# Performance work log

Hardware: AMD Instinct MI355X
Metric: run time of the kernel (lower is better)

## Reference

```python
import jax, jax.numpy as jnp
import numpy as np

D_MODEL = 1024
NUM_HEADS = 16
HEAD_DIM = D_MODEL // NUM_HEADS


def setup_inputs() -> dict:
    key = jax.random.key(0)
    ks = jax.random.split(key, 9)
    s = 1.0 / np.sqrt(D_MODEL)
    x = jax.random.normal(ks[0], (4, 2048, D_MODEL), dtype=jnp.float32)
    Wq = jax.random.uniform(ks[1], (D_MODEL, D_MODEL), jnp.float32, -s, s)
    bq = jax.random.uniform(ks[2], (D_MODEL,), jnp.float32, -s, s)
    Wk = jax.random.uniform(ks[3], (D_MODEL, D_MODEL), jnp.float32, -s, s)
    bk = jax.random.uniform(ks[4], (D_MODEL,), jnp.float32, -s, s)
    Wv = jax.random.uniform(ks[5], (D_MODEL, D_MODEL), jnp.float32, -s, s)
    bv = jax.random.uniform(ks[6], (D_MODEL,), jnp.float32, -s, s)
    Wo = jax.random.uniform(ks[7], (D_MODEL, D_MODEL), jnp.float32, -s, s)
    bo = jax.random.uniform(ks[8], (D_MODEL,), jnp.float32, -s, s)
    return {"x": x, "Wq": Wq, "bq": bq, "Wk": Wk, "bk": bk,
            "Wv": Wv, "bv": bv, "Wo": Wo, "bo": bo}


def reference(x, Wq, bq, Wk, bk, Wv, bv, Wo, bo):
    B, S, _ = x.shape
    H, Dh = NUM_HEADS, HEAD_DIM
    # projections (torch Linear: x @ W.T + b); split heads -> [B, H, S, Dh]
    q = (x @ Wq.T + bq).reshape(B, S, H, Dh).transpose(0, 2, 1, 3)
    k = (x @ Wk.T + bk).reshape(B, S, H, Dh).transpose(0, 2, 1, 3)
    v = (x @ Wv.T + bv).reshape(B, S, H, Dh).transpose(0, 2, 1, 3)
    scale = 1.0 / np.sqrt(Dh)
    scores = jnp.einsum("bhqd,bhkd->bhqk", q, k) * scale  # [B,H,S,S]
    attn = jax.nn.softmax(scores, axis=-1)
    out = jnp.einsum("bhqk,bhkd->bhqd", attn, v)  # [B,H,S,Dh]
    out = out.transpose(0, 2, 1, 3).reshape(B, S, H * Dh)
    return out @ Wo.T + bo
```

## Files before the change

kernel.cpp:

```cpp
#include <hip/hip_runtime.h>
#include <hip/hip_bf16.h>
#include <stdint.h>

typedef __hip_bfloat16 bf16;
typedef __attribute__((ext_vector_type(8))) short short8;
typedef __attribute__((ext_vector_type(4))) short short4v;
typedef __attribute__((ext_vector_type(4))) float f32x4;

#define MFMA16(a, b, c) __builtin_amdgcn_mfma_f32_16x16x32_bf16(a, b, c, 0, 0, 0)
#define LROW 144

static __device__ __forceinline__ short f2bf(float f) {
    bf16 h = __float2bfloat16(f);
    return *(short*)&h;
}

#define BAR_LGKM() asm volatile("s_waitcnt lgkmcnt(0)\ns_barrier" ::: "memory")
#define BAR_RAW()  asm volatile("s_barrier" ::: "memory")

__global__ __launch_bounds__(256) void cvt_f32_bf16(const float* __restrict__ s,
                                                    bf16* __restrict__ d, int n8) {
    int i = blockIdx.x * blockDim.x + threadIdx.x;
    if (i >= n8) return;
    f32x4 a0 = *(const f32x4*)(s + (size_t)i * 8);
    f32x4 a1 = *(const f32x4*)(s + (size_t)i * 8 + 4);
    short8 r;
#pragma unroll
    for (int j = 0; j < 4; ++j) {
        r[j] = f2bf(a0[j]);
        r[4 + j] = f2bf(a1[j]);
    }
    *(short8*)(d + (size_t)i * 8) = r;
}

template <int MODE, bool SCALE, bool AF32>
__global__ __launch_bounds__(256) void gemm128(const void* __restrict__ Araw,
                                               const void* __restrict__ Wraw,
                                               const float* __restrict__ bias,
                                               void* __restrict__ outraw) {
    __shared__ __align__(16) char As[128 * LROW];
    __shared__ __align__(16) char Bs[128 * LROW];
    const int t = threadIdx.x;
    const int lane = t & 63;
    const int w = t >> 6;
    const int m0 = blockIdx.x * 128;
    const int n0 = blockIdx.y * 128;
    const int wm = (w >> 1) * 64;
    const int wn = (w & 1) * 64;

    f32x4 acc[4][4] = {};
    const char* Ab = (const char*)Araw;
    const char* Wb = (const char*)Wraw;

    short8 av[4], wv[4];
    auto loadAB = [&](int k0) {
#pragma unroll
        for (int i = 0; i < 4; ++i) {
            int off = i * 4096 + t * 16;
            int row = off >> 7;
            int cb = off & 127;
            if (MODE == 3) {
                int gr = m0 + row;
                int bb = gr >> 11, ss = gr & 2047;
                int h = k0 >> 6;
                av[i] = *(const short8*)(Ab +
                        (((size_t)(bb * 16 + h) * 2048 + ss) * 64) * 2 + cb);
            } else if (AF32) {
                const char* s = Ab + (size_t)(m0 + row) * 4096 +
                                (size_t)k0 * 4 + cb * 2;
                f32x4 a0 = *(const f32x4*)s;
                f32x4 a1 = *(const f32x4*)(s + 16);
                short8 r;
#pragma unroll
                for (int j = 0; j < 4; ++j) { r[j] = f2bf(a0[j]); r[4+j] = f2bf(a1[j]); }
                av[i] = r;
            } else {
                av[i] = *(const short8*)(Ab + (size_t)(m0 + row) * 2048 +
                                         (size_t)k0 * 2 + cb);
            }
            if (AF32) {
                const char* s = Wb + (size_t)(n0 + row) * 4096 +
                                (size_t)k0 * 4 + cb * 2;
                f32x4 a0 = *(const f32x4*)s;
                f32x4 a1 = *(const f32x4*)(s + 16);
                short8 r;
#pragma unroll
                for (int j = 0; j < 4; ++j) { r[j] = f2bf(a0[j]); r[4+j] = f2bf(a1[j]); }
                wv[i] = r;
            } else {
                wv[i] = *(const short8*)(Wb + (size_t)(n0 + row) * 2048 +
                                         (size_t)k0 * 2 + cb);
            }
        }
    };

    loadAB(0);
    for (int k0 = 0; k0 < 1024; k0 += 64) {
#pragma unroll
        for (int i = 0; i < 4; ++i) {
            int off = i * 4096 + t * 16;
            int row = off >> 7, cb = off & 127;
            *(short8*)(As + row * LROW + cb) = av[i];
            *(short8*)(Bs + row * LROW + cb) = wv[i];
        }
        if (k0 < 960) loadAB(k0 + 64);
        BAR_LGKM();
#pragma unroll
        for (int kk = 0; kk < 2; ++kk) {
            short8 af[4], bfr[4];
#pragma unroll
            for (int m = 0; m < 4; ++m) {
                int row = wm + m * 16 + (lane & 15);
                af[m] = *(const short8*)(As + row * LROW + kk * 64 + (lane >> 4) * 16);
            }
#pragma unroll
            for (int n = 0; n < 4; ++n) {
                int row = wn + n * 16 + (lane & 15);
                bfr[n] = *(const short8*)(Bs + row * LROW + kk * 64 + (lane >> 4) * 16);
            }
#pragma unroll
            for (int m = 0; m < 4; ++m)
#pragma unroll
                for (int n = 0; n < 4; ++n)
                    acc[m][n] = MFMA16(af[m], bfr[n], acc[m][n]);
        }
        BAR_RAW();
    }

#pragma unroll
    for (int n = 0; n < 4; ++n) {
        int col = n0 + wn + n * 16 + (lane & 15);
        float bv = bias[col];
        int h = col >> 6, d = col & 63;
#pragma unroll
        for (int m = 0; m < 4; ++m) {
#pragma unroll
            for (int r = 0; r < 4; ++r) {
                int row = m0 + wm + m * 16 + (lane >> 4) * 4 + r;
                float v = acc[m][n][r] + bv;
                if (SCALE) v *= 0.18033688011112042f;
                if (MODE == 0) {
                    int b = row >> 11, s = row & 2047;
                    ((bf16*)outraw)[(((size_t)(b * 16 + h)) * 2048 + s) * 64 + d] =
                        __float2bfloat16(v);
                } else if (MODE == 1) {
                    int b = row >> 11, s = row & 2047;
                    ((bf16*)outraw)[(((size_t)(b * 16 + h)) * 64 + d) * 2048 + s] =
                        __float2bfloat16(v);
                } else {
                    ((float*)outraw)[(size_t)row * 1024 + col] = v;
                }
            }
        }
    }
}

__global__ __launch_bounds__(256) void flash_attn2(bf16* __restrict__ Q,
                                                   const bf16* __restrict__ K,
                                                   const bf16* __restrict__ Vt) {
    __shared__ __align__(16) char Kt[2][64 * LROW];
    __shared__ __align__(16) char Vs[2][64 * LROW];
    __shared__ __align__(16) char Ps[4 * 16 * LROW];

    const int t = threadIdx.x, lane = t & 63, w = t >> 6;
    const int bh = blockIdx.y;
    const int q0 = blockIdx.x * 64;
    const size_t base = (size_t)bh * 2048 * 64;

    const char* Qb = (const char*)(Q + base + (size_t)q0 * 64);
    const char* Kb = (const char*)(K + base);
    const char* Vb = (const char*)(Vt + base);

#pragma unroll
    for (int i = 0; i < 2; ++i) {
        int off = i * 4096 + t * 16;
        int row = off >> 7, cb = off & 127;
        short8 v = *(const short8*)(Qb + row * 128 + cb);
        *(short8*)(Ps + row * LROW + cb) = v;
    }
    __syncthreads();
    short8 qf[2];
#pragma unroll
    for (int kk = 0; kk < 2; ++kk) {
        int row = w * 16 + (lane & 15);
        qf[kk] = *(const short8*)(Ps + row * LROW + kk * 64 + (lane >> 4) * 16);
    }
    __syncthreads();

    float l = 0.f;
    f32x4 oacc[4];
#pragma unroll
    for (int n = 0; n < 4; ++n) oacc[n] = (f32x4){0.f, 0.f, 0.f, 0.f};

    char* Pw = Ps + w * (16 * LROW);

    const int off0 = t * 16, row0 = off0 >> 7, cb0 = off0 & 127;
    const int off1 = 4096 + t * 16, row1 = off1 >> 7, cb1 = off1 & 127;

    short8 kr0, kr1, vr0, vr1;
    auto LOADKV = [&](int kv0) {
        kr0 = *(const short8*)(Kb + (size_t)kv0 * 128 + row0 * 128 + cb0);
        kr1 = *(const short8*)(Kb + (size_t)kv0 * 128 + row1 * 128 + cb1);
        vr0 = *(const short8*)(Vb + (size_t)kv0 * 2 + row0 * 4096 + cb0);
        vr1 = *(const short8*)(Vb + (size_t)kv0 * 2 + row1 * 4096 + cb1);
    };
    LOADKV(0);

    for (int it = 0; it < 32; ++it) {
        char* Ktc = Kt[it & 1];
        char* Vsc = Vs[it & 1];
        *(short8*)(Ktc + row0 * LROW + cb0) = kr0;
        *(short8*)(Ktc + row1 * LROW + cb1) = kr1;
        *(short8*)(Vsc + row0 * LROW + cb0) = vr0;
        *(short8*)(Vsc + row1 * LROW + cb1) = vr1;
        if (it < 31) LOADKV((it + 1) * 64);
        BAR_LGKM();

        f32x4 sfT[4];
        __builtin_amdgcn_s_setprio(1);
#pragma unroll
        for (int n = 0; n < 4; ++n) {
            int row = n * 16 + (lane & 15);
            short8 kf0 = *(const short8*)(Ktc + row * LROW + (lane >> 4) * 16);
            short8 kf1 = *(const short8*)(Ktc + row * LROW + 64 + (lane >> 4) * 16);
            f32x4 z = {0.f, 0.f, 0.f, 0.f};
            sfT[n] = MFMA16(kf0, qf[0], z);
            sfT[n] = MFMA16(kf1, qf[1], sfT[n]);
        }
        __builtin_amdgcn_s_setprio(0);

#pragma unroll
        for (int n = 0; n < 4; ++n) {
            float p0 = exp2f(sfT[n][0]);
            float p1 = exp2f(sfT[n][1]);
            float p2 = exp2f(sfT[n][2]);
            float p3 = exp2f(sfT[n][3]);
            l += (p0 + p1) + (p2 + p3);
            short4v pk = {f2bf(p0), f2bf(p1), f2bf(p2), f2bf(p3)};
            *(short4v*)(Pw + (lane & 15) * LROW + n * 32 + (lane >> 4) * 8) = pk;
        }
        asm volatile("s_waitcnt lgkmcnt(0)" ::: "memory");

        short8 pa0 = *(const short8*)(Pw + (lane & 15) * LROW + (lane >> 4) * 16);
        short8 pa1 = *(const short8*)(Pw + (lane & 15) * LROW + 64 + (lane >> 4) * 16);
        __builtin_amdgcn_s_setprio(1);
#pragma unroll
        for (int n = 0; n < 4; ++n) {
            int row = n * 16 + (lane & 15);
            short8 vf0 = *(const short8*)(Vsc + row * LROW + (lane >> 4) * 16);
            short8 vf1 = *(const short8*)(Vsc + row * LROW + 64 + (lane >> 4) * 16);
            oacc[n] = MFMA16(pa0, vf0, oacc[n]);
            oacc[n] = MFMA16(pa1, vf1, oacc[n]);
        }
        __builtin_amdgcn_s_setprio(0);
    }

    l += __shfl_xor(l, 16, 64);
    l += __shfl_xor(l, 32, 64);
#pragma unroll
    for (int n = 0; n < 4; ++n) {
        int d = n * 16 + (lane & 15);
#pragma unroll
        for (int r = 0; r < 4; ++r) {
            float lr = __shfl(l, (lane >> 4) * 4 + r, 64);
            int srow = q0 + w * 16 + (lane >> 4) * 4 + r;
            Q[base + (size_t)srow * 64 + d] = __float2bfloat16(oacc[n][r] / lr);
        }
    }
}

extern "C" void kernel_launch(void* const* d_in, const int* in_sizes, int n_in,
                              void* d_out, int out_size, void* d_ws,
                              size_t ws_size, hipStream_t stream) {
    const float* x = (const float*)d_in[0];
    const float* Wq = (const float*)d_in[1];
    const float* bq = (const float*)d_in[2];
    const float* Wk = (const float*)d_in[3];
    const float* bk = (const float*)d_in[4];
    const float* Wv = (const float*)d_in[5];
    const float* bv = (const float*)d_in[6];
    const float* Wo = (const float*)d_in[7];
    const float* bo = (const float*)d_in[8];

    char* ws = (char*)d_ws;
    bf16* Qw = (bf16*)(ws);
    bf16* Kw = (bf16*)(ws + ((size_t)16 << 20));
    bf16* Vw = (bf16*)(ws + ((size_t)32 << 20));

    dim3 g(64, 8), blk(256);
    const bool fast = ws_size >= ((size_t)74 << 20);

    if (fast) {
        bf16* xb  = (bf16*)(ws + ((size_t)48 << 20));
        bf16* Wqb = (bf16*)(ws + ((size_t)66 << 20));
        bf16* Wkb = (bf16*)(ws + ((size_t)68 << 20));
        bf16* Wvb = (bf16*)(ws + ((size_t)70 << 20));
        bf16* Wob = (bf16*)(ws + ((size_t)72 << 20));
        cvt_f32_bf16<<<4096, 256, 0, stream>>>(x, xb, 1048576);
        cvt_f32_bf16<<<512, 256, 0, stream>>>(Wq, Wqb, 131072);
        cvt_f32_bf16<<<512, 256, 0, stream>>>(Wk, Wkb, 131072);
        cvt_f32_bf16<<<512, 256, 0, stream>>>(Wv, Wvb, 131072);
        cvt_f32_bf16<<<512, 256, 0, stream>>>(Wo, Wob, 131072);
        gemm128<0, true,  false><<<g, blk, 0, stream>>>(xb, Wqb, bq, Qw);
        gemm128<0, false, false><<<g, blk, 0, stream>>>(xb, Wkb, bk, Kw);
        gemm128<1, false, false><<<g, blk, 0, stream>>>(xb, Wvb, bv, Vw);
        flash_attn2<<<dim3(32, 64), blk, 0, stream>>>(Qw, Kw, Vw);
        gemm128<3, false, false><<<g, blk, 0, stream>>>(Qw, Wob, bo, d_out);
    } else {
        gemm128<0, true,  true><<<g, blk, 0, stream>>>(x, Wq, bq, Qw);
        gemm128<0, false, true><<<g, blk, 0, stream>>>(x, Wk, bk, Kw);
        gemm128<1, false, true><<<g, blk, 0, stream>>>(x, Wv, bv, Vw);
        flash_attn2<<<dim3(32, 64), blk, 0, stream>>>(Qw, Kw, Vw);
        gemm128<3, false, true><<<g, blk, 0, stream>>>(Qw, Wo, bo, d_out);
    }
}
```

Measured before the change: 249.9 us.

## Split KV across waves in attention and keep P in registers

The attention kernel now gives each wave 16 keys of every 64-key tile for all 64 queries, where before each wave owned 16 queries and covered all keys. Because of this, the exp'd scores feed a 16x16x16 MFMA straight from registers, with no LDS round trip for P. Partial outputs and row sums from the four waves are reduced through shared memory at the end. This cuts per-iteration LDS traffic and waits, and swaps in a raw exp2 builtin. In exchange it uses more accumulator registers (64 floats of oacc per lane), adds a multi-barrier epilogue reduction, and does half the K per MFMA instruction.

Result: no change. 247.0 us (median of 6 runs) (-1.1%).

```diff
diff --git a/kernel.cpp b/kernel.cpp
--- a/kernel.cpp
+++ b/kernel.cpp
@@ -9,6 +9,22 @@
 
 #define MFMA16(a, b, c) __builtin_amdgcn_mfma_f32_16x16x32_bf16(a, b, c, 0, 0, 0)
 #define LROW 144
+
+static __device__ __forceinline__ f32x4 MFMA16K16(short4v a, short4v b, f32x4 c) {
+#if __has_builtin(__builtin_amdgcn_mfma_f32_16x16x16bf16_1k)
+    return __builtin_amdgcn_mfma_f32_16x16x16bf16_1k(a, b, c, 0, 0, 0);
+#else
+    asm volatile("s_nop 1\nv_mfma_f32_16x16x16_bf16 %0, %1, %2, %0"
+                 : "+v"(c) : "v"(a), "v"(b));
+    return c;
+#endif
+}
+
+#if __has_builtin(__builtin_amdgcn_exp2f)
+#define EXP2(x) __builtin_amdgcn_exp2f(x)
+#else
+#define EXP2(x) exp2f(x)
+#endif
 
 static __device__ __forceinline__ short f2bf(float f) {
     bf16 h = __float2bfloat16(f);
@@ -155,14 +171,14 @@
     }
 }
 
-__global__ __launch_bounds__(256) void flash_attn2(bf16* __restrict__ Q,
+__global__ __launch_bounds__(256) void flash_attn4(bf16* __restrict__ Q,
                                                    const bf16* __restrict__ K,
                                                    const bf16* __restrict__ Vt) {
-    __shared__ __align__(16) char Kt[2][64 * LROW];
-    __shared__ __align__(16) char Vs[2][64 * LROW];
-    __shared__ __align__(16) char Ps[4 * 16 * LROW];
+    __shared__ __align__(16) char SMEM[2 * 2 * 64 * LROW];
+    __shared__ __align__(16) float lbuf[4 * 64];
 
     const int t = threadIdx.x, lane = t & 63, w = t >> 6;
+    const int c = lane & 15, g = lane >> 4;
     const int bh = blockIdx.y;
     const int q0 = blockIdx.x * 64;
     const size_t base = (size_t)bh * 2048 * 64;
@@ -170,29 +186,6 @@
     const char* Qb = (const char*)(Q + base + (size_t)q0 * 64);
     const char* Kb = (const char*)(K + base);
     const char* Vb = (const char*)(Vt + base);
-
-#pragma unroll
-    for (int i = 0; i < 2; ++i) {
-        int off = i * 4096 + t * 16;
-        int row = off >> 7, cb = off & 127;
-        short8 v = *(const short8*)(Qb + row * 128 + cb);
-        *(short8*)(Ps + row * LROW + cb) = v;
-    }
-    __syncthreads();
-    short8 qf[2];
-#pragma unroll
-    for (int kk = 0; kk < 2; ++kk) {
-        int row = w * 16 + (lane & 15);
-        qf[kk] = *(const short8*)(Ps + row * LROW + kk * 64 + (lane >> 4) * 16);
-    }
-    __syncthreads();
-
-    float l = 0.f;
-    f32x4 oacc[4];
-#pragma unroll
-    for (int n = 0; n < 4; ++n) oacc[n] = (f32x4){0.f, 0.f, 0.f, 0.f};
-
-    char* Pw = Ps + w * (16 * LROW);
 
     const int off0 = t * 16, row0 = off0 >> 7, cb0 = off0 & 127;
     const int off1 = 4096 + t * 16, row1 = off1 >> 7, cb1 = off1 & 127;
@@ -206,9 +199,34 @@
     };
     LOADKV(0);
 
+    {
+        short8 q8a = *(const short8*)(Qb + row0 * 128 + cb0);
+        short8 q8b = *(const short8*)(Qb + row1 * 128 + cb1);
+        *(short8*)(SMEM + row0 * LROW + cb0) = q8a;
+        *(short8*)(SMEM + row1 * LROW + cb1) = q8b;
+    }
+    __syncthreads();
+    short8 qf[4][2];
+#pragma unroll
+    for (int qb = 0; qb < 4; ++qb)
+#pragma unroll
+        for (int kk = 0; kk < 2; ++kk)
+            qf[qb][kk] = *(const short8*)(SMEM + (qb * 16 + c) * LROW +
+                                          kk * 64 + 16 * g);
+    __syncthreads();
+
+    float l_r[4] = {0.f, 0.f, 0.f, 0.f};
+    f32x4 oacc[4][4];
+#pragma unroll
+    for (int a = 0; a < 4; ++a)
+#pragma unroll
+        for (int b = 0; b < 4; ++b) oacc[a][b] = (f32x4){0.f, 0.f, 0.f, 0.f};
+
+    const int krow = (16 * w + c) * LROW + 16 * g;
+
     for (int it = 0; it < 32; ++it) {
-        char* Ktc = Kt[it & 1];
-        char* Vsc = Vs[it & 1];
+        char* Ktc = SMEM + (it & 1) * 9216;
+        char* Vsc = SMEM + 18432 + (it & 1) * 9216;
         *(short8*)(Ktc + row0 * LROW + cb0) = kr0;
         *(short8*)(Ktc + row1 * LROW + cb1) = kr1;
         *(short8*)(Vsc + row0 * LROW + cb0) = vr0;
@@ -216,55 +234,113 @@
         if (it < 31) LOADKV((it + 1) * 64);
         BAR_LGKM();
 
+        short8 kf0 = *(const short8*)(Ktc + krow);
+        short8 kf1 = *(const short8*)(Ktc + krow + 64);
         f32x4 sfT[4];
         __builtin_amdgcn_s_setprio(1);
 #pragma unroll
-        for (int n = 0; n < 4; ++n) {
-            int row = n * 16 + (lane & 15);
-            short8 kf0 = *(const short8*)(Ktc + row * LROW + (lane >> 4) * 16);
-            short8 kf1 = *(const short8*)(Ktc + row * LROW + 64 + (lane >> 4) * 16);
+        for (int qb = 0; qb < 4; ++qb) {
             f32x4 z = {0.f, 0.f, 0.f, 0.f};
-            sfT[n] = MFMA16(kf0, qf[0], z);
-            sfT[n] = MFMA16(kf1, qf[1], sfT[n]);
+            sfT[qb] = MFMA16(kf0, qf[qb][0], z);
+            sfT[qb] = MFMA16(kf1, qf[qb][1], sfT[qb]);
         }
         __builtin_amdgcn_s_setprio(0);
 
-#pragma unroll
-        for (int n = 0; n < 4; ++n) {
-            float p0 = exp2f(sfT[n][0]);
-            float p1 = exp2f(sfT[n][1]);
-            float p2 = exp2f(sfT[n][2]);
-            float p3 = exp2f(sfT[n][3]);
-            l += (p0 + p1) + (p2 + p3);
-            short4v pk = {f2bf(p0), f2bf(p1), f2bf(p2), f2bf(p3)};
-            *(short4v*)(Pw + (lane & 15) * LROW + n * 32 + (lane >> 4) * 8) = pk;
-        }
-        asm volatile("s_waitcnt lgkmcnt(0)" ::: "memory");
-
-        short8 pa0 = *(const short8*)(Pw + (lane & 15) * LROW + (lane >> 4) * 16);
-        short8 pa1 = *(const short8*)(Pw + (lane & 15) * LROW + 64 + (lane >> 4) * 16);
+        short4v pa[4];
+#pragma unroll
+        for (int qb = 0; qb < 4; ++qb) {
+            float p0 = EXP2(sfT[qb][0]);
+            float p1 = EXP2(sfT[qb][1]);
+            float p2 = EXP2(sfT[qb][2]);
+            float p3 = EXP2(sfT[qb][3]);
+            l_r[qb] += (p0 + p1) + (p2 + p3);
+            pa[qb] = (short4v){f2bf(p0), f2bf(p1), f2bf(p2), f2bf(p3)};
+        }
+
         __builtin_amdgcn_s_setprio(1);
 #pragma unroll
-        for (int n = 0; n < 4; ++n) {
-            int row = n * 16 + (lane & 15);
-            short8 vf0 = *(const short8*)(Vsc + row * LROW + (lane >> 4) * 16);
-            short8 vf1 = *(const short8*)(Vsc + row * LROW + 64 + (lane >> 4) * 16);
-            oacc[n] = MFMA16(pa0, vf0, oacc[n]);
-            oacc[n] = MFMA16(pa1, vf1, oacc[n]);
+        for (int db = 0; db < 4; ++db) {
+            short4v vf = *(const short4v*)(Vsc + (db * 16 + c) * LROW +
+                                           32 * w + 8 * g);
+#pragma unroll
+            for (int qb = 0; qb < 4; ++qb)
+                oacc[qb][db] = MFMA16K16(pa[qb], vf, oacc[qb][db]);
         }
         __builtin_amdgcn_s_setprio(0);
     }
 
-    l += __shfl_xor(l, 16, 64);
-    l += __shfl_xor(l, 32, 64);
-#pragma unroll
-    for (int n = 0; n < 4; ++n) {
-        int d = n * 16 + (lane & 15);
-#pragma unroll
-        for (int r = 0; r < 4; ++r) {
-            float lr = __shfl(l, (lane >> 4) * 4 + r, 64);
-            int srow = q0 + w * 16 + (lane >> 4) * 4 + r;
-            Q[base + (size_t)srow * 64 + d] = __float2bfloat16(oacc[n][r] / lr);
+    __syncthreads();
+
+#pragma unroll
+    for (int qb = 0; qb < 4; ++qb) {
+        l_r[qb] += __shfl_xor(l_r[qb], 16, 64);
+        l_r[qb] += __shfl_xor(l_r[qb], 32, 64);
+    }
+    if (lane < 16)
+#pragma unroll
+        for (int qb = 0; qb < 4; ++qb) lbuf[w * 64 + qb * 16 + lane] = l_r[qb];
+
+    float* red = (float*)SMEM;
+    if (w & 1) {
+        float* dst = red + (w >> 1) * 4096;
+#pragma unroll
+        for (int qb = 0; qb < 4; ++qb)
+#pragma unroll
+            for (int db = 0; db < 4; ++db)
+                *(f32x4*)(dst + qb * 1024 + g * 256 + (db * 16 + c) * 4) =
+                    oacc[qb][db];
+    }
+    __syncthreads();
+    if (!(w & 1)) {
+        const float* src = red + (w >> 1) * 4096;
+#pragma unroll
+        for (int qb = 0; qb < 4; ++qb)
+#pragma unroll
+            for (int db = 0; db < 4; ++db) {
+                f32x4 v = *(const f32x4*)(src + qb * 1024 + g * 256 +
+                                          (db * 16 + c) * 4);
+                oacc[qb][db] += v;
+            }
+    }
+    __syncthreads();
+    if (w == 2) {
+#pragma unroll
+        for (int qb = 0; qb < 4; ++qb)
+#pragma unroll
+            for (int db = 0; db < 4; ++db)
+                *(f32x4*)(red + qb * 1024 + g * 256 + (db * 16 + c) * 4) =
+                    oacc[qb][db];
+    }
+    __syncthreads();
+    if (w == 0) {
+#pragma unroll
+        for (int qb = 0; qb < 4; ++qb) {
+#pragma unroll
+            for (int db = 0; db < 4; ++db) {
+                f32x4 v = *(const f32x4*)(red + qb * 1024 + g * 256 +
+                                          (db * 16 + c) * 4);
+                oacc[qb][db] += v;
+            }
+        }
+#pragma unroll
+        for (int qb = 0; qb < 4; ++qb) {
+            float linv[4];
+#pragma unroll
+            for (int r = 0; r < 4; ++r) {
+                int q = qb * 16 + 4 * g + r;
+                float s = lbuf[q] + lbuf[64 + q] + lbuf[128 + q] + lbuf[192 + q];
+                linv[r] = 1.0f / s;
+            }
+#pragma unroll
+            for (int db = 0; db < 4; ++db) {
+#pragma unroll
+                for (int r = 0; r < 4; ++r) {
+                    int srow = q0 + qb * 16 + 4 * g + r;
+                    int d = db * 16 + c;
+                    Q[base + (size_t)srow * 64 + d] =
+                        __float2bfloat16(oacc[qb][db][r] * linv[r]);
+                }
+            }
         }
     }
 }
@@ -304,13 +380,13 @@
         gemm128<0, true,  false><<<g, blk, 0, stream>>>(xb, Wqb, bq, Qw);
         gemm128<0, false, false><<<g, blk, 0, stream>>>(xb, Wkb, bk, Kw);
         gemm128<1, false, false><<<g, blk, 0, stream>>>(xb, Wvb, bv, Vw);
-        flash_attn2<<<dim3(32, 64), blk, 0, stream>>>(Qw, Kw, Vw);
+        flash_attn4<<<dim3(32, 64), blk, 0, stream>>>(Qw, Kw, Vw);
         gemm128<3, false, false><<<g, blk, 0, stream>>>(Qw, Wob, bo, d_out);
     } else {
         gemm128<0, true,  true><<<g, blk, 0, stream>>>(x, Wq, bq, Qw);
         gemm128<0, false, true><<<g, blk, 0, stream>>>(x, Wk, bk, Kw);
         gemm128<1, false, true><<<g, blk, 0, stream>>>(x, Wv, bv, Vw);
-        flash_attn2<<<dim3(32, 64), blk, 0, stream>>>(Qw, Kw, Vw);
+        flash_attn4<<<dim3(32, 64), blk, 0, stream>>>(Qw, Kw, Vw);
         gemm128<3, false, true><<<g, blk, 0, stream>>>(Qw, Wo, bo, d_out);
     }
 }
```
